# Optimization experiments

Measured on AMD Instinct MI355X. Metric: run time of the kernel, lower is better.

The kernel has to match this reference:

```python
import jax, jax.numpy as jnp
import numpy as np

N = 50000      # nodes
D = 128        # in_dim
O = 128        # out_dim
MAX_DEG = 32   # degrees uniform in [0, MAX_DEG]


def setup_inputs() -> dict:
    rng = np.random.default_rng(0)
    deg = rng.integers(0, MAX_DEG + 1, size=N)          # includes deg==0 nodes
    dst = np.repeat(np.arange(N), deg)                  # target node per edge (grouped, like the buckets)
    E = dst.shape[0]                                    # ~800000
    src = rng.integers(0, N, size=E)                    # neighbor index per edge (flat neighbor_list)

    key = jax.random.key(0)
    k1, k2, k3, k4 = jax.random.split(key, 4)
    scale = jnp.float32(1.0 / np.sqrt(D))
    return {
        "x":  jax.random.normal(k1, (N, D), jnp.float32),
        "Wg": jax.random.normal(k2, (O, D), jnp.float32) * scale,  # global_lin.weight
        "Wl": jax.random.normal(k3, (O, D), jnp.float32) * scale,  # local_lin.weight
        "Ws": jax.random.normal(k4, (O, D), jnp.float32) * scale,  # self_lin.weight
        "b":  jnp.zeros((O,), jnp.float32),                        # bias param
        "src": jnp.asarray(src, jnp.int32),
        "dst": jnp.asarray(dst, jnp.int32),
        "deg": jnp.asarray(deg, jnp.int32),
    }


def reference(x, Wg, Wl, Ws, b, src, dst, deg):
    n = x.shape[0]
    # global branch: applied to every node
    g_out = x @ Wg.T                                           # [N, O]
    # mean-aggregate neighbor features (gather + segment-sum == the per-bucket view().mean())
    neigh_sum = jax.ops.segment_sum(x[src], dst, num_segments=n)   # [N, D]
    degf = jnp.maximum(deg, 1).astype(x.dtype)[:, None]
    neigh_mean = neigh_sum * (1.0 / degf)                       # [N, D]
    # local + self branches only for deg > 0 (deg==0 bucket keeps just global_out)
    mask = (deg > 0).astype(x.dtype)[:, None]                   # [N, 1]
    out = g_out + mask * (neigh_mean @ Wl.T + x @ Ws.T) + b
    # dropout is identity in eval mode; ELU activation
    return jax.nn.elu(out)
```

## Files before the change

kernel.cpp:

```cpp
#include <hip/hip_runtime.h>
#include <cstdint>
#include <cstddef>

#define GNPB 8
#define MNPB 16
#define GAST 264
#define DAST 136
#define VP_BLOCKS 16
#define VPG_BLOCKS 8

typedef __attribute__((ext_vector_type(8))) short bf16x8;
typedef __attribute__((ext_vector_type(4))) float f32x4;

static __device__ __forceinline__ unsigned short f2bf(float f) {
    unsigned int u = __builtin_bit_cast(unsigned int, f);
    u += 0x7fffu + ((u >> 16) & 1u);
    return (unsigned short)(u >> 16);
}
static __device__ __forceinline__ float bfhi(unsigned int u) { return __builtin_bit_cast(float, u & 0xFFFF0000u); }
static __device__ __forceinline__ float bflo(unsigned int u) { return __builtin_bit_cast(float, u << 16); }
static __device__ __forceinline__ void acc8(float* a, const uint4& v, unsigned m) {
    unsigned x0 = v.x & m, x1 = v.y & m, x2 = v.z & m, x3 = v.w & m;
    a[0] += bflo(x0); a[1] += bfhi(x0); a[2] += bflo(x1); a[3] += bfhi(x1);
    a[4] += bflo(x2); a[5] += bfhi(x2); a[6] += bflo(x3); a[7] += bfhi(x3);
}

__global__ __launch_bounds__(256)
void prep(const float* __restrict__ x, const float* __restrict__ Wg,
          const float* __restrict__ Wl, const float* __restrict__ Ws,
          const int* __restrict__ dst, const int* __restrict__ deg,
          unsigned short* __restrict__ Vp, unsigned short* __restrict__ Vpg,
          unsigned short* __restrict__ xb, int* __restrict__ blkoff,
          int* __restrict__ d0cnt, int* __restrict__ d0list,
          int total8, int nblk_g, int noffb, int ncmp, int E, int N) {
    const int bx = blockIdx.x, t = threadIdx.x;
    if (bx < VP_BLOCKS) {
        int gid = bx * 256 + t;
        if (gid < 4096) {
            int l = gid & 63, srow = (gid >> 6) & 7, g = gid >> 9;
            int o = g * 16 + (l & 15);
            int k = srow * 32 + (l >> 4) * 8;
            uint4 u;
            if (k < 128) {
                const float* pg = Wg + o * 128 + k;
                const float* ps = Ws + o * 128 + k;
                u.x = (unsigned)f2bf(pg[0]+ps[0]) | ((unsigned)f2bf(pg[1]+ps[1]) << 16);
                u.y = (unsigned)f2bf(pg[2]+ps[2]) | ((unsigned)f2bf(pg[3]+ps[3]) << 16);
                u.z = (unsigned)f2bf(pg[4]+ps[4]) | ((unsigned)f2bf(pg[5]+ps[5]) << 16);
                u.w = (unsigned)f2bf(pg[6]+ps[6]) | ((unsigned)f2bf(pg[7]+ps[7]) << 16);
            } else {
                const float* pl = Wl + o * 128 + (k - 128);
                u.x = (unsigned)f2bf(pl[0]) | ((unsigned)f2bf(pl[1]) << 16);
                u.y = (unsigned)f2bf(pl[2]) | ((unsigned)f2bf(pl[3]) << 16);
                u.z = (unsigned)f2bf(pl[4]) | ((unsigned)f2bf(pl[5]) << 16);
                u.w = (unsigned)f2bf(pl[6]) | ((unsigned)f2bf(pl[7]) << 16);
            }
            ((uint4*)Vp)[gid] = u;
        }
    } else if (bx < VP_BLOCKS + VPG_BLOCKS) {
        int gid = (bx - VP_BLOCKS) * 256 + t;
        if (gid < 2048) {
            int l = gid & 63, s = (gid >> 6) & 3, g = gid >> 8;
            int o = g * 16 + (l & 15);
            int k = s * 32 + (l >> 4) * 8;
            const float* p = Wg + o * 128 + k;
            uint4 u;
            u.x = (unsigned)f2bf(p[0]) | ((unsigned)f2bf(p[1]) << 16);
            u.y = (unsigned)f2bf(p[2]) | ((unsigned)f2bf(p[3]) << 16);
            u.z = (unsigned)f2bf(p[4]) | ((unsigned)f2bf(p[5]) << 16);
            u.w = (unsigned)f2bf(p[6]) | ((unsigned)f2bf(p[7]) << 16);
            ((uint4*)Vpg)[gid] = u;
        }
    } else if (bx < VP_BLOCKS + VPG_BLOCKS + noffb) {
        int b = (bx - VP_BLOCKS - VPG_BLOCKS) * 256 + t;
        if (b < nblk_g) {
            int target = b * GNPB;
            int lo = 0, hi = E;
            while (lo < hi) { int mid = (lo + hi) >> 1; if (dst[mid] < target) lo = mid + 1; else hi = mid; }
            blkoff[b] = lo;
        }
    } else if (bx < VP_BLOCKS + VPG_BLOCKS + noffb + ncmp) {
        int n = (bx - VP_BLOCKS - VPG_BLOCKS - noffb) * 256 + t;
        if (n < N && deg[n] == 0) {
            int i = atomicAdd(d0cnt, 1);
            d0list[i] = n;
        }
    } else {
        int gid = (bx - VP_BLOCKS - VPG_BLOCKS - noffb - ncmp) * 256 + t;
        if (gid < total8) {
            const float4* px = (const float4*)x + (size_t)gid * 2;
            float4 a = px[0], bq = px[1];
            uint4 u;
            u.x = (unsigned)f2bf(a.x)  | ((unsigned)f2bf(a.y)  << 16);
            u.y = (unsigned)f2bf(a.z)  | ((unsigned)f2bf(a.w)  << 16);
            u.z = (unsigned)f2bf(bq.x) | ((unsigned)f2bf(bq.y) << 16);
            u.w = (unsigned)f2bf(bq.z) | ((unsigned)f2bf(bq.w) << 16);
            ((uint4*)xb)[gid] = u;
        }
    }
}

__global__ __launch_bounds__(512, 7)
void gather(const unsigned short* __restrict__ xb, const int* __restrict__ src,
            const int* __restrict__ deg, const int* __restrict__ blkoff,
            unsigned short* __restrict__ M, int N) {
    const int t = threadIdx.x, wv = t >> 6, lane = t & 63;
    const int c = lane & 15, p = lane >> 4;
    const int base = blockIdx.x * GNPB;

    int dg8 = 0;
    if (lane < GNPB && base + lane < N) dg8 = deg[base + lane];
    int incl = dg8;
#pragma unroll
    for (int off = 1; off < GNPB; off <<= 1) {
        int v = __shfl_up(incl, off, 64);
        if (lane >= off) incl += v;
    }
    const int d = __shfl(dg8, wv, 64);
    const int s = blkoff[blockIdx.x] + __shfl(incl, wv, 64) - d;
    const int n = base + wv;
    if (n >= N) return;

    int idx = 0;
    if (lane < d) idx = src[s + lane];

    const uint4* x4 = (const uint4*)xb;
    int r0 = __shfl(idx, p, 64),      r1 = __shfl(idx, p + 4, 64);
    int r2 = __shfl(idx, p + 8, 64),  r3 = __shfl(idx, p + 12, 64);
    uint4 v0 = x4[(size_t)r0 * 16 + c], v1 = x4[(size_t)r1 * 16 + c];
    uint4 v2 = x4[(size_t)r2 * 16 + c], v3 = x4[(size_t)r3 * 16 + c];
    uint4 v4, v5, v6, v7;
    const bool two = (d > 16);
    if (two) {
        int e = 16 + p;
        int r4 = __shfl(idx, e, 64),      r5 = __shfl(idx, e + 4, 64);
        int r6 = __shfl(idx, e + 8, 64),  r7 = __shfl(idx, e + 12, 64);
        v4 = x4[(size_t)r4 * 16 + c]; v5 = x4[(size_t)r5 * 16 + c];
        v6 = x4[(size_t)r6 * 16 + c]; v7 = x4[(size_t)r7 * 16 + c];
    }
    float a[8] = {0,0,0,0,0,0,0,0};
    float b[8] = {0,0,0,0,0,0,0,0};
    acc8(a, v0, (p      < d) ? ~0u : 0u);
    acc8(b, v1, (p + 4  < d) ? ~0u : 0u);
    acc8(a, v2, (p + 8  < d) ? ~0u : 0u);
    acc8(b, v3, (p + 12 < d) ? ~0u : 0u);
    if (two) {
        int e = 16 + p;
        acc8(a, v4, (e      < d) ? ~0u : 0u);
        acc8(b, v5, (e + 4  < d) ? ~0u : 0u);
        acc8(a, v6, (e + 8  < d) ? ~0u : 0u);
        acc8(b, v7, (e + 12 < d) ? ~0u : 0u);
    }
#pragma unroll
    for (int i = 0; i < 8; ++i) a[i] += b[i];
#pragma unroll
    for (int i = 0; i < 8; ++i) {
        a[i] += __shfl_xor(a[i], 16, 64);
        a[i] += __shfl_xor(a[i], 32, 64);
    }
    if (p == 0) {
        float inv = (d > 0) ? 1.0f / (float)d : 0.0f;
        uint4 u;
        u.x = (unsigned)f2bf(a[0]*inv) | ((unsigned)f2bf(a[1]*inv) << 16);
        u.y = (unsigned)f2bf(a[2]*inv) | ((unsigned)f2bf(a[3]*inv) << 16);
        u.z = (unsigned)f2bf(a[4]*inv) | ((unsigned)f2bf(a[5]*inv) << 16);
        u.w = (unsigned)f2bf(a[6]*inv) | ((unsigned)f2bf(a[7]*inv) << 16);
        ((uint4*)M)[(size_t)n * 16 + c] = u;
    }
}

__global__ __launch_bounds__(256)
void gemm(const unsigned short* __restrict__ xb, const unsigned short* __restrict__ Mm,
          const unsigned short* __restrict__ Vp, const float* __restrict__ bias,
          float* __restrict__ out, int N) {
    __shared__ __align__(16) unsigned short As[MNPB * GAST];
    const int t = threadIdx.x, wv = t >> 6, lane = t & 63;
    const int c = lane & 15, quad = lane >> 4;
    const int base = blockIdx.x * MNPB;

#pragma unroll
    for (int it = 0; it < 2; ++it) {
        int f = it * 256 + t;
        int row = f >> 5, ch = f & 31;
        int grow = base + row; if (grow > N - 1) grow = N - 1;
        const unsigned short* gp = (ch < 16)
            ? xb + (size_t)grow * 128 + ch * 8
            : Mm + (size_t)grow * 128 + (ch - 16) * 8;
        uint4 val = *(const uint4*)gp;
        *(uint4*)(As + row * GAST + ch * 8) = val;
    }
    const int g0 = 2 * wv, g1 = 2 * wv + 1;
    const bf16x8* VB = (const bf16x8*)Vp;
    bf16x8 b0 = VB[(g0 * 8) * 64 + lane];
    bf16x8 b1 = VB[(g1 * 8) * 64 + lane];
    __syncthreads();

    f32x4 acc0 = (f32x4){0.f, 0.f, 0.f, 0.f};
    f32x4 acc1 = (f32x4){0.f, 0.f, 0.f, 0.f};
#pragma unroll
    for (int s2 = 0; s2 < 8; ++s2) {
        int sn = (s2 + 1) & 7;
        bf16x8 n0 = VB[(g0 * 8 + sn) * 64 + lane];
        bf16x8 n1 = VB[(g1 * 8 + sn) * 64 + lane];
        bf16x8 a0 = *(const bf16x8*)(As + c * GAST + s2 * 32 + quad * 8);
        acc0 = __builtin_amdgcn_mfma_f32_16x16x32_bf16(a0, b0, acc0, 0, 0, 0);
        acc1 = __builtin_amdgcn_mfma_f32_16x16x32_bf16(a0, b1, acc1, 0, 0, 0);
        b0 = n0; b1 = n1;
    }

    const int col0 = g0 * 16 + c, col1 = g1 * 16 + c;
    const float bv0 = bias[col0], bv1 = bias[col1];
#pragma unroll
    for (int reg = 0; reg < 4; ++reg) {
        int grow = base + quad * 4 + reg;
        if (grow < N) {
            float v0 = acc0[reg] + bv0;
            float v1 = acc1[reg] + bv1;
            out[(size_t)grow * 128 + col0] = (v0 > 0.f) ? v0 : __expf(v0) - 1.0f;
            out[(size_t)grow * 128 + col1] = (v1 > 0.f) ? v1 : __expf(v1) - 1.0f;
        }
    }
}

__global__ __launch_bounds__(256)
void degfix(const unsigned short* __restrict__ xb, const int* __restrict__ d0list,
            const int* __restrict__ d0cnt, const unsigned short* __restrict__ Vpg,
            const float* __restrict__ bias, float* __restrict__ out) {
    const int cnt = *d0cnt;
    const int base = blockIdx.x * 16;
    if (base >= cnt) return;
    __shared__ __align__(16) unsigned short As[16 * DAST];
    const int t = threadIdx.x, wv = t >> 6, lane = t & 63;
    const int c = lane & 15, quad = lane >> 4;

    {
        int row = t >> 4, ch = t & 15;
        int i = base + row; if (i > cnt - 1) i = cnt - 1;
        int node = d0list[i];
        uint4 val = *(const uint4*)(xb + (size_t)node * 128 + ch * 8);
        *(uint4*)(As + row * DAST + ch * 8) = val;
    }
    const int g0 = 2 * wv, g1 = 2 * wv + 1;
    const bf16x8* VB = (const bf16x8*)Vpg;
    bf16x8 b0 = VB[(g0 * 4) * 64 + lane];
    bf16x8 b1 = VB[(g1 * 4) * 64 + lane];
    __syncthreads();

    f32x4 acc0 = (f32x4){0.f,0.f,0.f,0.f};
    f32x4 acc1 = (f32x4){0.f,0.f,0.f,0.f};
#pragma unroll
    for (int s2 = 0; s2 < 4; ++s2) {
        int sn = (s2 + 1) & 3;
        bf16x8 n0 = VB[(g0 * 4 + sn) * 64 + lane];
        bf16x8 n1 = VB[(g1 * 4 + sn) * 64 + lane];
        bf16x8 a0 = *(const bf16x8*)(As + c * DAST + s2 * 32 + quad * 8);
        acc0 = __builtin_amdgcn_mfma_f32_16x16x32_bf16(a0, b0, acc0, 0, 0, 0);
        acc1 = __builtin_amdgcn_mfma_f32_16x16x32_bf16(a0, b1, acc1, 0, 0, 0);
        b0 = n0; b1 = n1;
    }

    const int col0 = g0 * 16 + c, col1 = g1 * 16 + c;
    const float bv0 = bias[col0], bv1 = bias[col1];
#pragma unroll
    for (int reg = 0; reg < 4; ++reg) {
        int i = base + quad * 4 + reg;
        if (i < cnt) {
            int n = d0list[i];
            float v0 = acc0[reg] + bv0;
            float v1 = acc1[reg] + bv1;
            out[(size_t)n * 128 + col0] = (v0 > 0.f) ? v0 : __expf(v0) - 1.0f;
            out[(size_t)n * 128 + col1] = (v1 > 0.f) ? v1 : __expf(v1) - 1.0f;
        }
    }
}

extern "C" void kernel_launch(void* const* d_in, const int* in_sizes, int n_in,
                              void* d_out, int out_size, void* d_ws, size_t ws_size,
                              hipStream_t stream) {
    const float* x  = (const float*)d_in[0];
    const float* Wg = (const float*)d_in[1];
    const float* Wl = (const float*)d_in[2];
    const float* Ws = (const float*)d_in[3];
    const float* b  = (const float*)d_in[4];
    const int*   src = (const int*)d_in[5];
    const int*   dst = (const int*)d_in[6];
    const int*   deg = (const int*)d_in[7];
    const int E = in_sizes[5];
    const int N = in_sizes[7];
    float* out = (float*)d_out;

    const size_t NB = (size_t)N * 128 * 2;
    unsigned short* Vp     = (unsigned short*)d_ws;
    unsigned short* Vpg    = (unsigned short*)((char*)d_ws + 65536);
    int*            blkoff = (int*)((char*)d_ws + 98304);
    int*            d0cnt  = (int*)((char*)d_ws + 131072);
    int*            d0list = (int*)((char*)d_ws + 131328);
    unsigned short* xb     = (unsigned short*)((char*)d_ws + 335872);
    unsigned short* Mm     = (unsigned short*)((char*)d_ws + 335872 + NB);

    const int nblk_g = (N + GNPB - 1) / GNPB;
    const int noffb  = (nblk_g + 255) / 256;
    const int ncmp   = (N + 255) / 256;
    const int total8 = N * 16;
    const int nconv  = (total8 + 255) / 256;

    hipMemsetAsync(d0cnt, 0, sizeof(int), stream);
    prep<<<dim3(VP_BLOCKS + VPG_BLOCKS + noffb + ncmp + nconv), dim3(256), 0, stream>>>(
        x, Wg, Wl, Ws, dst, deg, Vp, Vpg, xb, blkoff, d0cnt, d0list,
        total8, nblk_g, noffb, ncmp, E, N);
    gather<<<dim3(nblk_g), dim3(512), 0, stream>>>(xb, src, deg, blkoff, Mm, N);
    gemm<<<dim3((N + MNPB - 1) / MNPB), dim3(256), 0, stream>>>(xb, Mm, Vp, b, out, N);
    degfix<<<dim3((N + 15) / 16), dim3(256), 0, stream>>>(xb, d0list, d0cnt, Vpg, b, out);
}
```

Measured before the change: 148.6 us.

## Fold degree-zero fixup into GEMM kernel with per-block local compaction

Removes the separate degfix kernel, the global atomic compaction of degree-zero nodes in prep, and the memset. Extra blocks appended to the GEMM grid each scan a range of 512 nodes, compact the degree-zero ones into shared memory, and compute the global-only product for them. The main GEMM blocks now skip writing rows whose degree is zero. This saves a launch and a memset and drops the global atomics, but the extra blocks loop serially over their local list and add reads of deg.

```diff
diff --git a/kernel.cpp b/kernel.cpp
--- a/kernel.cpp
+++ b/kernel.cpp
@@ -5,7 +5,7 @@
 #define GNPB 8
 #define MNPB 16
 #define GAST 264
-#define DAST 136
+#define DFRNG 512
 #define VP_BLOCKS 16
 #define VPG_BLOCKS 8
 
@@ -28,11 +28,10 @@
 __global__ __launch_bounds__(256)
 void prep(const float* __restrict__ x, const float* __restrict__ Wg,
           const float* __restrict__ Wl, const float* __restrict__ Ws,
-          const int* __restrict__ dst, const int* __restrict__ deg,
+          const int* __restrict__ dst,
           unsigned short* __restrict__ Vp, unsigned short* __restrict__ Vpg,
           unsigned short* __restrict__ xb, int* __restrict__ blkoff,
-          int* __restrict__ d0cnt, int* __restrict__ d0list,
-          int total8, int nblk_g, int noffb, int ncmp, int E, int N) {
+          int total8, int nblk_g, int noffb, int E) {
     const int bx = blockIdx.x, t = threadIdx.x;
     if (bx < VP_BLOCKS) {
         int gid = bx * 256 + t;
@@ -79,14 +78,8 @@
             while (lo < hi) { int mid = (lo + hi) >> 1; if (dst[mid] < target) lo = mid + 1; else hi = mid; }
             blkoff[b] = lo;
         }
-    } else if (bx < VP_BLOCKS + VPG_BLOCKS + noffb + ncmp) {
-        int n = (bx - VP_BLOCKS - VPG_BLOCKS - noffb) * 256 + t;
-        if (n < N && deg[n] == 0) {
-            int i = atomicAdd(d0cnt, 1);
-            d0list[i] = n;
-        }
     } else {
-        int gid = (bx - VP_BLOCKS - VPG_BLOCKS - noffb - ncmp) * 256 + t;
+        int gid = (bx - VP_BLOCKS - VPG_BLOCKS - noffb) * 256 + t;
         if (gid < total8) {
             const float4* px = (const float4*)x + (size_t)gid * 2;
             float4 a = px[0], bq = px[1];
@@ -171,13 +164,73 @@
 
 __global__ __launch_bounds__(256)
 void gemm(const unsigned short* __restrict__ xb, const unsigned short* __restrict__ Mm,
-          const unsigned short* __restrict__ Vp, const float* __restrict__ bias,
-          float* __restrict__ out, int N) {
+          const int* __restrict__ deg, const unsigned short* __restrict__ Vp,
+          const unsigned short* __restrict__ Vpg, const float* __restrict__ bias,
+          float* __restrict__ out, int N, int ngemm) {
     __shared__ __align__(16) unsigned short As[MNPB * GAST];
     const int t = threadIdx.x, wv = t >> 6, lane = t & 63;
     const int c = lane & 15, quad = lane >> 4;
+    const int g0 = 2 * wv, g1 = 2 * wv + 1;
+    const int col0 = g0 * 16 + c, col1 = g1 * 16 + c;
+    const float bv0 = bias[col0], bv1 = bias[col1];
+
+    if (blockIdx.x >= ngemm) {
+        __shared__ int nds[DFRNG];
+        __shared__ int ncnt;
+        const int rb = (blockIdx.x - ngemm) * DFRNG;
+        if (t == 0) ncnt = 0;
+        __syncthreads();
+#pragma unroll
+        for (int i = 0; i < DFRNG / 256; ++i) {
+            int n = rb + i * 256 + t;
+            if (n < N && deg[n] == 0) nds[atomicAdd(&ncnt, 1)] = n;
+        }
+        __syncthreads();
+        const int cnt = ncnt;
+        if (cnt == 0) return;
+        const bf16x8* VB = (const bf16x8*)Vpg;
+        for (int base = 0; base < cnt; base += 16) {
+            {
+                int row = t >> 4, ch = t & 15;
+                int i = base + row; if (i > cnt - 1) i = cnt - 1;
+                int node = nds[i];
+                uint4 val = *(const uint4*)(xb + (size_t)node * 128 + ch * 8);
+                *(uint4*)(As + row * GAST + ch * 8) = val;
+            }
+            bf16x8 b0 = VB[(g0 * 4) * 64 + lane];
+            bf16x8 b1 = VB[(g1 * 4) * 64 + lane];
+            __syncthreads();
+            f32x4 acc0 = (f32x4){0.f,0.f,0.f,0.f};
+            f32x4 acc1 = (f32x4){0.f,0.f,0.f,0.f};
+#pragma unroll
+            for (int s2 = 0; s2 < 4; ++s2) {
+                int sn = (s2 + 1) & 3;
+                bf16x8 n0 = VB[(g0 * 4 + sn) * 64 + lane];
+                bf16x8 n1 = VB[(g1 * 4 + sn) * 64 + lane];
+                bf16x8 a0 = *(const bf16x8*)(As + c * GAST + s2 * 32 + quad * 8);
+                acc0 = __builtin_amdgcn_mfma_f32_16x16x32_bf16(a0, b0, acc0, 0, 0, 0);
+                acc1 = __builtin_amdgcn_mfma_f32_16x16x32_bf16(a0, b1, acc1, 0, 0, 0);
+                b0 = n0; b1 = n1;
+            }
+#pragma unroll
+            for (int reg = 0; reg < 4; ++reg) {
+                int i = base + quad * 4 + reg;
+                if (i < cnt) {
+                    int n = nds[i];
+                    float v0 = acc0[reg] + bv0;
+                    float v1 = acc1[reg] + bv1;
+                    out[(size_t)n * 128 + col0] = (v0 > 0.f) ? v0 : __expf(v0) - 1.0f;
+                    out[(size_t)n * 128 + col1] = (v1 > 0.f) ? v1 : __expf(v1) - 1.0f;
+                }
+            }
+            __syncthreads();
+        }
+        return;
+    }
+
+    __shared__ unsigned char srowok[MNPB];
     const int base = blockIdx.x * MNPB;
-
+    if (t < MNPB) srowok[t] = (base + t < N && deg[base + t] > 0) ? 1 : 0;
 #pragma unroll
     for (int it = 0; it < 2; ++it) {
         int f = it * 256 + t;
@@ -189,7 +242,6 @@
         uint4 val = *(const uint4*)gp;
         *(uint4*)(As + row * GAST + ch * 8) = val;
     }
-    const int g0 = 2 * wv, g1 = 2 * wv + 1;
     const bf16x8* VB = (const bf16x8*)Vp;
     bf16x8 b0 = VB[(g0 * 8) * 64 + lane];
     bf16x8 b1 = VB[(g1 * 8) * 64 + lane];
@@ -208,68 +260,15 @@
         b0 = n0; b1 = n1;
     }
 
-    const int col0 = g0 * 16 + c, col1 = g1 * 16 + c;
-    const float bv0 = bias[col0], bv1 = bias[col1];
 #pragma unroll
     for (int reg = 0; reg < 4; ++reg) {
-        int grow = base + quad * 4 + reg;
-        if (grow < N) {
+        int lrow = quad * 4 + reg;
+        int grow = base + lrow;
+        if (grow < N && srowok[lrow]) {
             float v0 = acc0[reg] + bv0;
             float v1 = acc1[reg] + bv1;
             out[(size_t)grow * 128 + col0] = (v0 > 0.f) ? v0 : __expf(v0) - 1.0f;
             out[(size_t)grow * 128 + col1] = (v1 > 0.f) ? v1 : __expf(v1) - 1.0f;
-        }
-    }
-}
-
-__global__ __launch_bounds__(256)
-void degfix(const unsigned short* __restrict__ xb, const int* __restrict__ d0list,
-            const int* __restrict__ d0cnt, const unsigned short* __restrict__ Vpg,
-            const float* __restrict__ bias, float* __restrict__ out) {
-    const int cnt = *d0cnt;
-    const int base = blockIdx.x * 16;
-    if (base >= cnt) return;
-    __shared__ __align__(16) unsigned short As[16 * DAST];
-    const int t = threadIdx.x, wv = t >> 6, lane = t & 63;
-    const int c = lane & 15, quad = lane >> 4;
-
-    {
-        int row = t >> 4, ch = t & 15;
-        int i = base + row; if (i > cnt - 1) i = cnt - 1;
-        int node = d0list[i];
-        uint4 val = *(const uint4*)(xb + (size_t)node * 128 + ch * 8);
-        *(uint4*)(As + row * DAST + ch * 8) = val;
-    }
-    const int g0 = 2 * wv, g1 = 2 * wv + 1;
-    const bf16x8* VB = (const bf16x8*)Vpg;
-    bf16x8 b0 = VB[(g0 * 4) * 64 + lane];
-    bf16x8 b1 = VB[(g1 * 4) * 64 + lane];
-    __syncthreads();
-
-    f32x4 acc0 = (f32x4){0.f,0.f,0.f,0.f};
-    f32x4 acc1 = (f32x4){0.f,0.f,0.f,0.f};
-#pragma unroll
-    for (int s2 = 0; s2 < 4; ++s2) {
-        int sn = (s2 + 1) & 3;
-        bf16x8 n0 = VB[(g0 * 4 + sn) * 64 + lane];
-        bf16x8 n1 = VB[(g1 * 4 + sn) * 64 + lane];
-        bf16x8 a0 = *(const bf16x8*)(As + c * DAST + s2 * 32 + quad * 8);
-        acc0 = __builtin_amdgcn_mfma_f32_16x16x32_bf16(a0, b0, acc0, 0, 0, 0);
-        acc1 = __builtin_amdgcn_mfma_f32_16x16x32_bf16(a0, b1, acc1, 0, 0, 0);
-        b0 = n0; b1 = n1;
-    }
-
-    const int col0 = g0 * 16 + c, col1 = g1 * 16 + c;
-    const float bv0 = bias[col0], bv1 = bias[col1];
-#pragma unroll
-    for (int reg = 0; reg < 4; ++reg) {
-        int i = base + quad * 4 + reg;
-        if (i < cnt) {
-            int n = d0list[i];
-            float v0 = acc0[reg] + bv0;
-            float v1 = acc1[reg] + bv1;
-            out[(size_t)n * 128 + col0] = (v0 > 0.f) ? v0 : __expf(v0) - 1.0f;
-            out[(size_t)n * 128 + col1] = (v1 > 0.f) ? v1 : __expf(v1) - 1.0f;
         }
     }
 }
@@ -293,22 +292,18 @@
     unsigned short* Vp     = (unsigned short*)d_ws;
     unsigned short* Vpg    = (unsigned short*)((char*)d_ws + 65536);
     int*            blkoff = (int*)((char*)d_ws + 98304);
-    int*            d0cnt  = (int*)((char*)d_ws + 131072);
-    int*            d0list = (int*)((char*)d_ws + 131328);
-    unsigned short* xb     = (unsigned short*)((char*)d_ws + 335872);
-    unsigned short* Mm     = (unsigned short*)((char*)d_ws + 335872 + NB);
+    unsigned short* xb     = (unsigned short*)((char*)d_ws + 131072);
+    unsigned short* Mm     = (unsigned short*)((char*)d_ws + 131072 + NB);
 
     const int nblk_g = (N + GNPB - 1) / GNPB;
     const int noffb  = (nblk_g + 255) / 256;
-    const int ncmp   = (N + 255) / 256;
     const int total8 = N * 16;
     const int nconv  = (total8 + 255) / 256;
-
-    hipMemsetAsync(d0cnt, 0, sizeof(int), stream);
-    prep<<<dim3(VP_BLOCKS + VPG_BLOCKS + noffb + ncmp + nconv), dim3(256), 0, stream>>>(
-        x, Wg, Wl, Ws, dst, deg, Vp, Vpg, xb, blkoff, d0cnt, d0list,
-        total8, nblk_g, noffb, ncmp, E, N);
+    const int ngemm  = (N + MNPB - 1) / MNPB;
+    const int ndeg   = (N + DFRNG - 1) / DFRNG;
+
+    prep<<<dim3(VP_BLOCKS + VPG_BLOCKS + noffb + nconv), dim3(256), 0, stream>>>(
+        x, Wg, Wl, Ws, dst, Vp, Vpg, xb, blkoff, total8, nblk_g, noffb, E);
     gather<<<dim3(nblk_g), dim3(512), 0, stream>>>(xb, src, deg, blkoff, Mm, N);
-    gemm<<<dim3((N + MNPB - 1) / MNPB), dim3(256), 0, stream>>>(xb, Mm, Vp, b, out, N);
-    degfix<<<dim3((N + 15) / 16), dim3(256), 0, stream>>>(xb, d0list, d0cnt, Vpg, b, out);
-}
+    gemm<<<dim3(ngemm + ndeg), dim3(256), 0, stream>>>(xb, Mm, deg, Vp, Vpg, b, out, N, ngemm);
+}
```

Result: faster. 137.9 us (-7.2%).
